# Optimization experiments

Measured on AMD Instinct MI355X. Metric: run time of the kernel, lower is better.

Reference implementation:

```python
import jax, jax.numpy as jnp
import numpy as np

N_NODES = 50000
N_EDGES = 800000
IN_DIM = 128
HID = 64
HEADS = 4
SLOPE = 0.01


def edge_softmax(e, dst, n):
    # e: [E, H] logits, softmax over edges sharing the same destination node
    m = jax.ops.segment_max(e, dst, num_segments=n)          # [N, H]
    ex = jnp.exp(e - m[dst])                                 # [E, H]
    s = jax.ops.segment_sum(ex, dst, num_segments=n)         # [N, H]
    return ex / s[dst]


def gat_conv(h, src, dst, W, attn_l, attn_r, bias, n, heads, out_dim):
    ft = (h @ W).reshape(n, heads, out_dim)                  # [N, H, D]
    el = jnp.sum(ft * attn_l, axis=-1)                       # [N, H]
    er = jnp.sum(ft * attn_r, axis=-1)                       # [N, H]
    e = jax.nn.leaky_relu(el[src] + er[dst], SLOPE)          # [E, H]
    a = edge_softmax(e, dst, n)                              # [E, H]
    msg = ft[src] * a[:, :, None]                            # [E, H, D]
    out = jax.ops.segment_sum(msg, dst, num_segments=n)      # [N, H, D]
    return out + bias.reshape(1, heads, out_dim)


def setup_inputs() -> dict:
    key = jax.random.key(0)
    ks = jax.random.split(key, 12)
    inputs = jax.random.normal(ks[0], (N_NODES, IN_DIM), dtype=jnp.float32)
    src = jax.random.randint(ks[1], (N_EDGES,), 0, N_NODES, dtype=jnp.int32)
    dst = jax.random.randint(ks[2], (N_EDGES,), 0, N_NODES, dtype=jnp.int32)
    s1 = 1.0 / np.sqrt(IN_DIM)
    W1 = jax.random.normal(ks[3], (IN_DIM, HEADS * HID), dtype=jnp.float32) * s1
    al1 = jax.random.normal(ks[4], (HEADS, HID), dtype=jnp.float32) * 0.1
    ar1 = jax.random.normal(ks[5], (HEADS, HID), dtype=jnp.float32) * 0.1
    b1 = jnp.zeros((HEADS * HID,), dtype=jnp.float32)
    s2 = 1.0 / np.sqrt(HEADS * HID)
    W2 = jax.random.normal(ks[6], (HEADS * HID, HID), dtype=jnp.float32) * s2
    al2 = jax.random.normal(ks[7], (1, HID), dtype=jnp.float32) * 0.1
    ar2 = jax.random.normal(ks[8], (1, HID), dtype=jnp.float32) * 0.1
    b2 = jnp.zeros((HID,), dtype=jnp.float32)
    return {"inputs": inputs, "src": src, "dst": dst,
            "W1": W1, "al1": al1, "ar1": ar1, "b1": b1,
            "W2": W2, "al2": al2, "ar2": ar2, "b2": b2}


def reference(inputs, src, dst, W1, al1, ar1, b1, W2, al2, ar2, b2):
    # layer 1: multi-head, activation elu, flatten heads
    h = gat_conv(inputs, src, dst, W1, al1, ar1, b1, N_NODES, HEADS, HID)
    h = jax.nn.elu(h).reshape(N_NODES, HEADS * HID)
    # layer 2 (last): single head
    h = gat_conv(h, src, dst, W2, al2, ar2, b2, N_NODES, 1, HID)
    h = jax.nn.elu(h).reshape(N_NODES, HID)
    return h
```

## Files before the change

### kernel.cpp

```cpp
#include <hip/hip_runtime.h>
#include <hip/hip_bf16.h>
#include <math.h>

#define N_NODES 50000
#define N_EDGES 800000
#define IN_DIM 128
#define HID 64
#define HEADS 4

typedef unsigned short ushort_t;
typedef __attribute__((ext_vector_type(8))) short bf16x8;
typedef __attribute__((ext_vector_type(4))) float f32x4;

static __device__ __forceinline__ ushort_t f2bf(float f) {
  __hip_bfloat16 b = __float2bfloat16(f);
  return *(ushort_t*)&b;
}
static __device__ __forceinline__ float bflo(unsigned d) {
  union { unsigned u; float f; } c; c.u = d << 16; return c.f;
}
static __device__ __forceinline__ float bfhi(unsigned d) {
  union { unsigned u; float f; } c; c.u = d & 0xffff0000u; return c.f;
}
static __device__ __forceinline__ unsigned packbf(float lo, float hi) {
  return (unsigned)f2bf(lo) | ((unsigned)f2bf(hi) << 16);
}
static __device__ __forceinline__ float lrelu(float x) {
  return (x > 0.f) ? x : 0.01f * x;
}

__global__ __launch_bounds__(256) void k_cvt_hist(const float* __restrict__ w1,
                                                  const float* __restrict__ w2,
                                                  ushort_t* __restrict__ bpk1,
                                                  ushort_t* __restrict__ bpk2,
                                                  const int* __restrict__ dst,
                                                  int* __restrict__ cnt) {
  constexpr int NP1 = 4096;
  constexpr int NP2 = 2048;
  constexpr int CVT_BLK = (NP1 + NP2) / 256;
  int bid = blockIdx.x;
  if (bid < CVT_BLK) {
    int t = bid * 256 + threadIdx.x;
    if (t < NP1) {
      int l = t & 63, rem = t >> 6;
      int kk = rem & 3, ct = (rem >> 2) & 3, hh = rem >> 4;
      int kb = kk * 32 + (l >> 4) * 8;
      int col = hh * 64 + ct * 16 + (l & 15);
      ushort_t v[8];
      #pragma unroll
      for (int j = 0; j < 8; ++j) v[j] = f2bf(w1[(kb + j) * 256 + col]);
      *(uint4*)&bpk1[t * 8] = *(uint4*)v;
    } else {
      int u = t - NP1;
      int l = u & 63, rem = u >> 6;
      int kk = rem & 7, ct = rem >> 3;
      int kb = kk * 32 + (l >> 4) * 8;
      int col = ct * 16 + (l & 15);
      ushort_t v[8];
      #pragma unroll
      for (int j = 0; j < 8; ++j) v[j] = f2bf(w2[(kb + j) * 64 + col]);
      *(uint4*)&bpk2[u * 8] = *(uint4*)v;
    }
  } else {
    int e = (bid - CVT_BLK) * 256 + threadIdx.x;
    if (e < N_EDGES) atomicAdd(&cnt[dst[e]], 1);
  }
}

__global__ __launch_bounds__(512) void k_scan_gemm1(const int* __restrict__ cnt,
                                                    int* __restrict__ offp,
                                                    int* __restrict__ bsum,
                                                    const float* __restrict__ A,
                                                    const ushort_t* __restrict__ Bpk,
                                                    ushort_t* __restrict__ C,
                                                    const float* __restrict__ al,
                                                    const float* __restrict__ ar,
                                                    float* __restrict__ el,
                                                    float* __restrict__ er, int M) {
  __shared__ char smraw[128 * 40 * 2];
  const int tid = threadIdx.x;
  if (blockIdx.x < 49) {
    int* lds = (int*)smraw;
    int i = blockIdx.x * 1024 + tid * 2;
    int v0 = (i < N_NODES) ? cnt[i] : 0;
    int v1 = (i + 1 < N_NODES) ? cnt[i + 1] : 0;
    int t = v0 + v1;
    lds[tid] = t;
    __syncthreads();
    for (int s = 1; s < 512; s <<= 1) {
      int u = (tid >= s) ? lds[tid - s] : 0;
      __syncthreads();
      lds[tid] += u;
      __syncthreads();
    }
    int excl = lds[tid] - t;
    if (i < N_NODES) offp[i] = excl;
    if (i + 1 < N_NODES) offp[i + 1] = excl + v0;
    if (tid == 511) bsum[blockIdx.x] = lds[511];
    return;
  }
  ushort_t (*As)[40] = (ushort_t(*)[40])smraw;
  const int m0 = (blockIdx.x - 49) * 128;
  const int w = tid >> 6, l = tid & 63;
  const int hh = w >> 1, rh = (w & 1) * 64;
  const int lr = l & 15, lk = l >> 4;
  f32x4 acc[4][4] = {};

  #pragma unroll
  for (int kk = 0; kk < 4; ++kk) {
    int k0 = kk * 32;
    {
      int r = tid >> 2, kc = (tid & 3) * 8;
      float4 va = make_float4(0.f, 0.f, 0.f, 0.f), vb = va;
      if (m0 + r < M) {
        va = *(const float4*)&A[(size_t)(m0 + r) * IN_DIM + k0 + kc];
        vb = *(const float4*)&A[(size_t)(m0 + r) * IN_DIM + k0 + kc + 4];
      }
      uint4 p;
      p.x = packbf(va.x, va.y); p.y = packbf(va.z, va.w);
      p.z = packbf(vb.x, vb.y); p.w = packbf(vb.z, vb.w);
      *(uint4*)&As[r][kc] = p;
    }
    __syncthreads();
    bf16x8 a[4];
    #pragma unroll
    for (int rt = 0; rt < 4; ++rt) a[rt] = *(const bf16x8*)&As[rh + rt * 16 + lr][lk * 8];
    #pragma unroll
    for (int ct = 0; ct < 4; ++ct) {
      bf16x8 b = ((const bf16x8*)Bpk)[((hh * 4 + ct) * 4 + kk) * 64 + l];
      #pragma unroll
      for (int rt = 0; rt < 4; ++rt)
        acc[rt][ct] = __builtin_amdgcn_mfma_f32_16x16x32_bf16(a[rt], b, acc[rt][ct], 0, 0, 0);
    }
    __syncthreads();
  }
  float ala[4], ara[4];
  #pragma unroll
  for (int ct = 0; ct < 4; ++ct) {
    ala[ct] = al[hh * 64 + ct * 16 + lr];
    ara[ct] = ar[hh * 64 + ct * 16 + lr];
  }
  #pragma unroll
  for (int rt = 0; rt < 4; ++rt)
    #pragma unroll
    for (int j = 0; j < 4; ++j) {
      float pel = 0.f, per = 0.f;
      #pragma unroll
      for (int ct = 0; ct < 4; ++ct) {
        float v = acc[rt][ct][j];
        pel = fmaf(v, ala[ct], pel);
        per = fmaf(v, ara[ct], per);
      }
      #pragma unroll
      for (int o = 1; o <= 8; o <<= 1) {
        pel += __shfl_xor(pel, o);
        per += __shfl_xor(per, o);
      }
      int row = m0 + rh + rt * 16 + lk * 4 + j;
      if (lr == 0 && row < M) { el[row * 4 + hh] = pel; er[row * 4 + hh] = per; }
    }
  #pragma unroll
  for (int rt = 0; rt < 4; ++rt)
    #pragma unroll
    for (int ct = 0; ct < 4; ++ct)
      #pragma unroll
      for (int j = 0; j < 4; ++j) {
        int row = m0 + rh + rt * 16 + lk * 4 + j;
        if (row < M) C[(size_t)row * 256 + hh * 64 + ct * 16 + lr] = f2bf(acc[rt][ct][j]);
      }
}

__global__ __launch_bounds__(256) void k_off_place(const int* __restrict__ offp,
                                                   const int* __restrict__ bsum,
                                                   int* __restrict__ off,
                                                   const int* __restrict__ src,
                                                   const int* __restrict__ dst,
                                                   int* __restrict__ cnt2,
                                                   int* __restrict__ ssrc) {
  __shared__ int pref[64];
  const int tid = threadIdx.x;
  const int bid = blockIdx.x;
  if (bid < 49) {
    if (tid < 64) {
      int v = (tid < bid) ? bsum[tid] : 0;
      #pragma unroll
      for (int o = 1; o < 64; o <<= 1) v += __shfl_xor(v, o);
      if (tid == 0) pref[0] = v;
    }
    __syncthreads();
    int e0 = pref[0];
    int i = bid * 1024 + tid * 4;
    if (i + 3 < N_NODES) {
      int4 q = *(const int4*)&offp[i];
      *(int4*)&off[i] = make_int4(q.x + e0, q.y + e0, q.z + e0, q.w + e0);
    } else {
      if (i < N_NODES) off[i] = offp[i] + e0;
      if (i + 1 < N_NODES) off[i + 1] = offp[i + 1] + e0;
      if (i + 2 < N_NODES) off[i + 2] = offp[i + 2] + e0;
      if (i + 3 < N_NODES) off[i + 3] = offp[i + 3] + e0;
    }
    if (bid == 0 && tid == 0) off[N_NODES] = N_EDGES;
    return;
  }
  if (tid < 64) {
    int v = (tid < 49) ? bsum[tid] : 0;
    int orig = v;
    #pragma unroll
    for (int o = 1; o < 64; o <<= 1) { int u = __shfl_up(v, o); if (tid >= o) v += u; }
    pref[tid] = v - orig;
  }
  __syncthreads();
  int e = (bid - 49) * 256 + tid;
  if (e < N_EDGES) {
    int d = dst[e];
    int p = atomicAdd(&cnt2[d], 1);
    ssrc[offp[d] + pref[d >> 10] + p] = src[e];
  }
}

__global__ __launch_bounds__(256) void agg4f_k(const ushort_t* __restrict__ ftb,
                                               const float* __restrict__ el,
                                               const float* __restrict__ er,
                                               const int* __restrict__ off,
                                               const int* __restrict__ ssrc,
                                               const float* __restrict__ bias,
                                               ushort_t* __restrict__ outb) {
  __shared__ float wl[4][64][4];
  __shared__ int srcl[4][64];
  int wv = threadIdx.x >> 6, lane = threadIdx.x & 63;
  int n = blockIdx.x * 4 + wv;
  if (n >= N_NODES) return;
  int s0 = off[n], s1 = off[n + 1];
  int half = lane >> 5, sl = lane & 31;
  int head = sl >> 3;
  const float4* el4 = (const float4*)el;
  float4 erv = ((const float4*)er)[n];
  float4 sum = make_float4(0.f, 0.f, 0.f, 0.f);
  float acc[8] = {};
  for (int c = s0; c < s1; c += 64) {
    int e = c + lane;
    float4 ex = make_float4(0.f, 0.f, 0.f, 0.f);
    int s = 0;
    if (e < s1) {
      s = ssrc[e];
      float4 q = el4[s];
      ex.x = __expf(lrelu(q.x + erv.x));
      ex.y = __expf(lrelu(q.y + erv.y));
      ex.z = __expf(lrelu(q.z + erv.z));
      ex.w = __expf(lrelu(q.w + erv.w));
      sum.x += ex.x; sum.y += ex.y; sum.z += ex.z; sum.w += ex.w;
    }
    srcl[wv][lane] = s;
    *(float4*)&wl[wv][lane][0] = ex;
    int cend = (c + 64 < s1) ? c + 64 : s1;
    #pragma unroll 4
    for (int i = c; i < cend; i += 2) {
      int e2 = i + half;
      if (e2 < cend) {
        int idx = e2 - c;
        int ss = srcl[wv][idx];
        float w = wl[wv][idx][head];
        uint4 u = *(const uint4*)&ftb[ss * 256 + sl * 8];
        acc[0] = fmaf(w, bflo(u.x), acc[0]);
        acc[1] = fmaf(w, bfhi(u.x), acc[1]);
        acc[2] = fmaf(w, bflo(u.y), acc[2]);
        acc[3] = fmaf(w, bfhi(u.y), acc[3]);
        acc[4] = fmaf(w, bflo(u.z), acc[4]);
        acc[5] = fmaf(w, bfhi(u.z), acc[5]);
        acc[6] = fmaf(w, bflo(u.w), acc[6]);
        acc[7] = fmaf(w, bfhi(u.w), acc[7]);
      }
    }
  }
  #pragma unroll
  for (int o = 1; o <= 32; o <<= 1) {
    sum.x += __shfl_xor(sum.x, o); sum.y += __shfl_xor(sum.y, o);
    sum.z += __shfl_xor(sum.z, o); sum.w += __shfl_xor(sum.w, o);
  }
  #pragma unroll
  for (int j = 0; j < 8; ++j) acc[j] += __shfl_xor(acc[j], 32);
  if (half == 0) {
    float sd = (head == 0) ? sum.x : (head == 1) ? sum.y : (head == 2) ? sum.z : sum.w;
    float rsv = (s1 > s0) ? 1.f / sd : 0.f;
    float4 b0 = ((const float4*)bias)[sl * 2];
    float4 b1 = ((const float4*)bias)[sl * 2 + 1];
    float o[8] = {fmaf(acc[0], rsv, b0.x), fmaf(acc[1], rsv, b0.y),
                  fmaf(acc[2], rsv, b0.z), fmaf(acc[3], rsv, b0.w),
                  fmaf(acc[4], rsv, b1.x), fmaf(acc[5], rsv, b1.y),
                  fmaf(acc[6], rsv, b1.z), fmaf(acc[7], rsv, b1.w)};
    #pragma unroll
    for (int j = 0; j < 8; ++j) o[j] = (o[j] > 0.f) ? o[j] : expm1f(o[j]);
    uint4 p;
    p.x = packbf(o[0], o[1]); p.y = packbf(o[2], o[3]);
    p.z = packbf(o[4], o[5]); p.w = packbf(o[6], o[7]);
    *(uint4*)&outb[n * 256 + sl * 8] = p;
  }
}

__global__ __launch_bounds__(512) void gemm2_mfma(const ushort_t* __restrict__ A,
                                                  const ushort_t* __restrict__ Bpk,
                                                  ushort_t* __restrict__ C,
                                                  const float* __restrict__ al,
                                                  const float* __restrict__ ar,
                                                  float* __restrict__ el,
                                                  float* __restrict__ er, int M) {
  __shared__ ushort_t As[128][40];
  const int tid = threadIdx.x;
  const int m0 = blockIdx.x * 128;
  const int w = tid >> 6, l = tid & 63;
  const int lr = l & 15, lk = l >> 4;
  f32x4 acc[4] = {};

  #pragma unroll
  for (int kk = 0; kk < 8; ++kk) {
    int k0 = kk * 32;
    {
      int r = tid >> 2, kc = (tid & 3) * 8;
      uint4 v = make_uint4(0, 0, 0, 0);
      if (m0 + r < M) v = *(const uint4*)&A[(size_t)(m0 + r) * 256 + k0 + kc];
      *(uint4*)&As[r][kc] = v;
    }
    __syncthreads();
    bf16x8 a = *(const bf16x8*)&As[w * 16 + lr][lk * 8];
    #pragma unroll
    for (int ct = 0; ct < 4; ++ct) {
      bf16x8 b = ((const bf16x8*)Bpk)[(ct * 8 + kk) * 64 + l];
      acc[ct] = __builtin_amdgcn_mfma_f32_16x16x32_bf16(a, b, acc[ct], 0, 0, 0);
    }
    __syncthreads();
  }
  float ala[4], ara[4];
  #pragma unroll
  for (int ct = 0; ct < 4; ++ct) {
    ala[ct] = al[ct * 16 + lr];
    ara[ct] = ar[ct * 16 + lr];
  }
  #pragma unroll
  for (int j = 0; j < 4; ++j) {
    float pel = 0.f, per = 0.f;
    #pragma unroll
    for (int ct = 0; ct < 4; ++ct) {
      float v = acc[ct][j];
      pel = fmaf(v, ala[ct], pel);
      per = fmaf(v, ara[ct], per);
    }
    #pragma unroll
    for (int o = 1; o <= 8; o <<= 1) {
      pel += __shfl_xor(pel, o);
      per += __shfl_xor(per, o);
    }
    int row = m0 + w * 16 + lk * 4 + j;
    if (lr == 0 && row < M) { el[row] = pel; er[row] = per; }
  }
  #pragma unroll
  for (int ct = 0; ct < 4; ++ct)
    #pragma unroll
    for (int j = 0; j < 4; ++j) {
      int row = m0 + w * 16 + lk * 4 + j;
      if (row < M) C[(size_t)row * 64 + ct * 16 + lr] = f2bf(acc[ct][j]);
    }
}

__global__ __launch_bounds__(256) void agg1f_k(const ushort_t* __restrict__ ftb,
                                               const float* __restrict__ el,
                                               const float* __restrict__ er,
                                               const int* __restrict__ off,
                                               const int* __restrict__ ssrc,
                                               const float* __restrict__ bias,
                                               float* __restrict__ out) {
  __shared__ float wl[4][64];
  __shared__ int srcl[4][64];
  int wv = threadIdx.x >> 6, lane = threadIdx.x & 63;
  int n = blockIdx.x * 4 + wv;
  if (n >= N_NODES) return;
  int s0 = off[n], s1 = off[n + 1];
  int g = lane >> 3, cg = lane & 7;
  float erv = er[n];
  float sum = 0.f;
  float acc[8] = {};
  for (int c = s0; c < s1; c += 64) {
    int e = c + lane;
    float ex = 0.f;
    int s = 0;
    if (e < s1) {
      s = ssrc[e];
      ex = __expf(lrelu(el[s] + erv));
      sum += ex;
    }
    srcl[wv][lane] = s;
    wl[wv][lane] = ex;
    int cend = (c + 64 < s1) ? c + 64 : s1;
    #pragma unroll 2
    for (int i = c; i < cend; i += 8) {
      int e2 = i + g;
      if (e2 < cend) {
        int idx = e2 - c;
        int ss = srcl[wv][idx];
        float w = wl[wv][idx];
        uint4 u = *(const uint4*)&ftb[ss * 64 + cg * 8];
        acc[0] = fmaf(w, bflo(u.x), acc[0]);
        acc[1] = fmaf(w, bfhi(u.x), acc[1]);
        acc[2] = fmaf(w, bflo(u.y), acc[2]);
        acc[3] = fmaf(w, bfhi(u.y), acc[3]);
        acc[4] = fmaf(w, bflo(u.z), acc[4]);
        acc[5] = fmaf(w, bfhi(u.z), acc[5]);
        acc[6] = fmaf(w, bflo(u.w), acc[6]);
        acc[7] = fmaf(w, bfhi(u.w), acc[7]);
      }
    }
  }
  #pragma unroll
  for (int o = 1; o <= 32; o <<= 1) sum += __shfl_xor(sum, o);
  #pragma unroll
  for (int o = 8; o <= 32; o <<= 1)
    #pragma unroll
    for (int j = 0; j < 8; ++j) acc[j] += __shfl_xor(acc[j], o);
  if (g == 0) {
    float rsv = (s1 > s0) ? 1.f / sum : 0.f;
    float4 b0 = ((const float4*)bias)[cg * 2];
    float4 b1 = ((const float4*)bias)[cg * 2 + 1];
    float o[8] = {fmaf(acc[0], rsv, b0.x), fmaf(acc[1], rsv, b0.y),
                  fmaf(acc[2], rsv, b0.z), fmaf(acc[3], rsv, b0.w),
                  fmaf(acc[4], rsv, b1.x), fmaf(acc[5], rsv, b1.y),
                  fmaf(acc[6], rsv, b1.z), fmaf(acc[7], rsv, b1.w)};
    #pragma unroll
    for (int j = 0; j < 8; ++j) o[j] = (o[j] > 0.f) ? o[j] : expm1f(o[j]);
    float4* out4 = (float4*)out;
    out4[(size_t)n * 16 + cg * 2]     = make_float4(o[0], o[1], o[2], o[3]);
    out4[(size_t)n * 16 + cg * 2 + 1] = make_float4(o[4], o[5], o[6], o[7]);
  }
}

extern "C" void kernel_launch(void* const* d_in, const int* in_sizes, int n_in,
                              void* d_out, int out_size, void* d_ws, size_t ws_size,
                              hipStream_t stream) {
  const float* x   = (const float*)d_in[0];
  const int*   src = (const int*)d_in[1];
  const int*   dst = (const int*)d_in[2];
  const float* W1  = (const float*)d_in[3];
  const float* al1 = (const float*)d_in[4];
  const float* ar1 = (const float*)d_in[5];
  const float* b1  = (const float*)d_in[6];
  const float* W2  = (const float*)d_in[7];
  const float* al2 = (const float*)d_in[8];
  const float* ar2 = (const float*)d_in[9];
  const float* b2  = (const float*)d_in[10];
  float* out = (float*)d_out;

  char* ws = (char*)d_ws;
  size_t wo = 0;
  auto alloc = [&](size_t b) { void* p = ws + wo; wo = (wo + b + 255) & ~(size_t)255; return p; };
  ushort_t* ft1b = (ushort_t*)alloc((size_t)N_NODES * 256 * 2);
  ushort_t* h1b  = (ushort_t*)alloc((size_t)N_NODES * 256 * 2);
  ushort_t* bpk1 = (ushort_t*)alloc((size_t)IN_DIM * 256 * 2);
  ushort_t* bpk2 = (ushort_t*)alloc((size_t)256 * 64 * 2);
  float* el1 = (float*)alloc((size_t)N_NODES * 4 * 4);
  float* er1 = (float*)alloc((size_t)N_NODES * 4 * 4);
  int*   off = (int*)alloc((size_t)(N_NODES + 1) * 4);
  int*   offp= (int*)alloc((size_t)N_NODES * 4);
  int*   cntp= (int*)alloc((size_t)2 * N_NODES * 4);
  int*   bsum= (int*)alloc(256);
  int*   ssrc= (int*)alloc((size_t)N_EDGES * 4);
  int* cnt  = cntp;
  int* cnt2 = cntp + N_NODES;
  ushort_t* ft2b = ft1b;
  float* el2 = el1, *er2 = er1;

  hipMemsetAsync(cntp, 0, (size_t)2 * N_NODES * 4, stream);
  k_cvt_hist<<<24 + 3125, 256, 0, stream>>>(W1, W2, bpk1, bpk2, dst, cnt);
  k_scan_gemm1<<<49 + 391, 512, 0, stream>>>(cnt, offp, bsum,
                                             x, bpk1, ft1b, al1, ar1, el1, er1, N_NODES);
  k_off_place<<<49 + 3125, 256, 0, stream>>>(offp, bsum, off, src, dst, cnt2, ssrc);
  agg4f_k<<<(N_NODES + 3) / 4, 256, 0, stream>>>(ft1b, el1, er1, off, ssrc, b1, h1b);
  gemm2_mfma<<<391, 512, 0, stream>>>(h1b, bpk2, ft2b, al2, ar2, el2, er2, N_NODES);
  agg1f_k<<<(N_NODES + 3) / 4, 256, 0, stream>>>(ft2b, el2, er2, off, ssrc, b2, out);
}
```

Measured before the change: 228.3 us.

## Fuse preprocessing and first GEMM into persistent kernel with grid barriers

Replaces three launches (weight conversion plus histogram, scan plus GEMM1, offset plus placement) with one persistent 512-block kernel that uses software grid barriers between phases. The GEMM1 tile shrinks to 32 rows with 256 threads, so it can interleave with edge placement. The scan is reworked to 4 elements per thread. The aim is to remove kernel launch gaps and tail effects. In exchange it adds spin-barrier overhead and relies on all 512 blocks being co-resident.

```diff
diff --git a/kernel.cpp b/kernel.cpp
--- a/kernel.cpp
+++ b/kernel.cpp
@@ -7,6 +7,7 @@
 #define IN_DIM 128
 #define HID 64
 #define HEADS 4
+#define MEGA_NB 512
 
 typedef unsigned short ushort_t;
 typedef __attribute__((ext_vector_type(8))) short bf16x8;
@@ -29,192 +30,188 @@
   return (x > 0.f) ? x : 0.01f * x;
 }
 
-__global__ __launch_bounds__(256) void k_cvt_hist(const float* __restrict__ w1,
-                                                  const float* __restrict__ w2,
-                                                  ushort_t* __restrict__ bpk1,
-                                                  ushort_t* __restrict__ bpk2,
-                                                  const int* __restrict__ dst,
-                                                  int* __restrict__ cnt) {
-  constexpr int NP1 = 4096;
-  constexpr int NP2 = 2048;
-  constexpr int CVT_BLK = (NP1 + NP2) / 256;
-  int bid = blockIdx.x;
-  if (bid < CVT_BLK) {
-    int t = bid * 256 + threadIdx.x;
-    if (t < NP1) {
-      int l = t & 63, rem = t >> 6;
-      int kk = rem & 3, ct = (rem >> 2) & 3, hh = rem >> 4;
-      int kb = kk * 32 + (l >> 4) * 8;
-      int col = hh * 64 + ct * 16 + (l & 15);
-      ushort_t v[8];
-      #pragma unroll
-      for (int j = 0; j < 8; ++j) v[j] = f2bf(w1[(kb + j) * 256 + col]);
-      *(uint4*)&bpk1[t * 8] = *(uint4*)v;
+static __device__ __forceinline__ void grid_barrier(unsigned* bar, unsigned nb) {
+  __syncthreads();
+  if (threadIdx.x == 0) {
+    __threadfence();
+    __hip_atomic_fetch_add(bar, 1u, __ATOMIC_ACQ_REL, __HIP_MEMORY_SCOPE_AGENT);
+    while (__hip_atomic_load(bar, __ATOMIC_ACQUIRE, __HIP_MEMORY_SCOPE_AGENT) < nb)
+      __builtin_amdgcn_s_sleep(8);
+    __threadfence();
+  }
+  __syncthreads();
+}
+
+__global__ __launch_bounds__(256, 2) void k_mega(
+    const float* __restrict__ w1, const float* __restrict__ w2,
+    ushort_t* __restrict__ bpk1, ushort_t* __restrict__ bpk2,
+    const int* __restrict__ dst, const int* __restrict__ src,
+    int* __restrict__ cnt, int* __restrict__ cnt2, unsigned* __restrict__ bar,
+    int* __restrict__ offp, int* __restrict__ bsum, int* __restrict__ off,
+    int* __restrict__ ssrc,
+    const float* __restrict__ A, ushort_t* __restrict__ C,
+    const float* __restrict__ al, const float* __restrict__ ar,
+    float* __restrict__ el, float* __restrict__ er) {
+  __shared__ char smraw[2816];
+  const int tid = threadIdx.x;
+  const unsigned nb = gridDim.x;
+
+  for (int u = blockIdx.x; u < 24 + 3125; u += MEGA_NB) {
+    if (u < 24) {
+      int t = u * 256 + tid;
+      if (t < 4096) {
+        int l = t & 63, rem = t >> 6;
+        int kk = rem & 3, ct = (rem >> 2) & 3, hh = rem >> 4;
+        int kb = kk * 32 + (l >> 4) * 8;
+        int col = hh * 64 + ct * 16 + (l & 15);
+        ushort_t v[8];
+        #pragma unroll
+        for (int j = 0; j < 8; ++j) v[j] = f2bf(w1[(kb + j) * 256 + col]);
+        *(uint4*)&bpk1[t * 8] = *(uint4*)v;
+      } else {
+        int q = t - 4096;
+        int l = q & 63, rem = q >> 6;
+        int kk = rem & 7, ct = rem >> 3;
+        int kb = kk * 32 + (l >> 4) * 8;
+        int col = ct * 16 + (l & 15);
+        ushort_t v[8];
+        #pragma unroll
+        for (int j = 0; j < 8; ++j) v[j] = f2bf(w2[(kb + j) * 64 + col]);
+        *(uint4*)&bpk2[q * 8] = *(uint4*)v;
+      }
     } else {
-      int u = t - NP1;
-      int l = u & 63, rem = u >> 6;
-      int kk = rem & 7, ct = rem >> 3;
-      int kb = kk * 32 + (l >> 4) * 8;
-      int col = ct * 16 + (l & 15);
-      ushort_t v[8];
-      #pragma unroll
-      for (int j = 0; j < 8; ++j) v[j] = f2bf(w2[(kb + j) * 64 + col]);
-      *(uint4*)&bpk2[u * 8] = *(uint4*)v;
-    }
-  } else {
-    int e = (bid - CVT_BLK) * 256 + threadIdx.x;
-    if (e < N_EDGES) atomicAdd(&cnt[dst[e]], 1);
-  }
-}
-
-__global__ __launch_bounds__(512) void k_scan_gemm1(const int* __restrict__ cnt,
-                                                    int* __restrict__ offp,
-                                                    int* __restrict__ bsum,
-                                                    const float* __restrict__ A,
-                                                    const ushort_t* __restrict__ Bpk,
-                                                    ushort_t* __restrict__ C,
-                                                    const float* __restrict__ al,
-                                                    const float* __restrict__ ar,
-                                                    float* __restrict__ el,
-                                                    float* __restrict__ er, int M) {
-  __shared__ char smraw[128 * 40 * 2];
-  const int tid = threadIdx.x;
-  if (blockIdx.x < 49) {
+      int e = (u - 24) * 256 + tid;
+      if (e < N_EDGES) atomicAdd(&cnt[dst[e]], 1);
+    }
+  }
+  grid_barrier(&bar[0], nb);
+
+  for (int u = blockIdx.x; u < 49; u += MEGA_NB) {
     int* lds = (int*)smraw;
-    int i = blockIdx.x * 1024 + tid * 2;
-    int v0 = (i < N_NODES) ? cnt[i] : 0;
-    int v1 = (i + 1 < N_NODES) ? cnt[i + 1] : 0;
-    int t = v0 + v1;
+    int i = u * 1024 + tid * 4;
+    int v0 = 0, v1 = 0, v2 = 0, v3 = 0;
+    if (i + 3 < N_NODES) {
+      int4 q = *(const int4*)&cnt[i];
+      v0 = q.x; v1 = q.y; v2 = q.z; v3 = q.w;
+    } else {
+      if (i < N_NODES) v0 = cnt[i];
+      if (i + 1 < N_NODES) v1 = cnt[i + 1];
+      if (i + 2 < N_NODES) v2 = cnt[i + 2];
+      if (i + 3 < N_NODES) v3 = cnt[i + 3];
+    }
+    int t = v0 + v1 + v2 + v3;
     lds[tid] = t;
     __syncthreads();
-    for (int s = 1; s < 512; s <<= 1) {
-      int u = (tid >= s) ? lds[tid - s] : 0;
+    for (int s = 1; s < 256; s <<= 1) {
+      int u2 = (tid >= s) ? lds[tid - s] : 0;
       __syncthreads();
-      lds[tid] += u;
+      lds[tid] += u2;
       __syncthreads();
     }
     int excl = lds[tid] - t;
     if (i < N_NODES) offp[i] = excl;
     if (i + 1 < N_NODES) offp[i + 1] = excl + v0;
-    if (tid == 511) bsum[blockIdx.x] = lds[511];
-    return;
-  }
-  ushort_t (*As)[40] = (ushort_t(*)[40])smraw;
-  const int m0 = (blockIdx.x - 49) * 128;
-  const int w = tid >> 6, l = tid & 63;
-  const int hh = w >> 1, rh = (w & 1) * 64;
-  const int lr = l & 15, lk = l >> 4;
-  f32x4 acc[4][4] = {};
-
-  #pragma unroll
-  for (int kk = 0; kk < 4; ++kk) {
-    int k0 = kk * 32;
-    {
-      int r = tid >> 2, kc = (tid & 3) * 8;
-      float4 va = make_float4(0.f, 0.f, 0.f, 0.f), vb = va;
-      if (m0 + r < M) {
-        va = *(const float4*)&A[(size_t)(m0 + r) * IN_DIM + k0 + kc];
-        vb = *(const float4*)&A[(size_t)(m0 + r) * IN_DIM + k0 + kc + 4];
-      }
-      uint4 p;
-      p.x = packbf(va.x, va.y); p.y = packbf(va.z, va.w);
-      p.z = packbf(vb.x, vb.y); p.w = packbf(vb.z, vb.w);
-      *(uint4*)&As[r][kc] = p;
-    }
+    if (i + 2 < N_NODES) offp[i + 2] = excl + v0 + v1;
+    if (i + 3 < N_NODES) offp[i + 3] = excl + v0 + v1 + v2;
+    if (tid == 255) bsum[u] = lds[255];
     __syncthreads();
-    bf16x8 a[4];
-    #pragma unroll
-    for (int rt = 0; rt < 4; ++rt) a[rt] = *(const bf16x8*)&As[rh + rt * 16 + lr][lk * 8];
-    #pragma unroll
-    for (int ct = 0; ct < 4; ++ct) {
-      bf16x8 b = ((const bf16x8*)Bpk)[((hh * 4 + ct) * 4 + kk) * 64 + l];
-      #pragma unroll
-      for (int rt = 0; rt < 4; ++rt)
-        acc[rt][ct] = __builtin_amdgcn_mfma_f32_16x16x32_bf16(a[rt], b, acc[rt][ct], 0, 0, 0);
-    }
-    __syncthreads();
-  }
-  float ala[4], ara[4];
-  #pragma unroll
-  for (int ct = 0; ct < 4; ++ct) {
-    ala[ct] = al[hh * 64 + ct * 16 + lr];
-    ara[ct] = ar[hh * 64 + ct * 16 + lr];
-  }
-  #pragma unroll
-  for (int rt = 0; rt < 4; ++rt)
-    #pragma unroll
-    for (int j = 0; j < 4; ++j) {
-      float pel = 0.f, per = 0.f;
-      #pragma unroll
-      for (int ct = 0; ct < 4; ++ct) {
-        float v = acc[rt][ct][j];
-        pel = fmaf(v, ala[ct], pel);
-        per = fmaf(v, ara[ct], per);
-      }
-      #pragma unroll
-      for (int o = 1; o <= 8; o <<= 1) {
-        pel += __shfl_xor(pel, o);
-        per += __shfl_xor(per, o);
-      }
-      int row = m0 + rh + rt * 16 + lk * 4 + j;
-      if (lr == 0 && row < M) { el[row * 4 + hh] = pel; er[row * 4 + hh] = per; }
-    }
-  #pragma unroll
-  for (int rt = 0; rt < 4; ++rt)
-    #pragma unroll
-    for (int ct = 0; ct < 4; ++ct)
-      #pragma unroll
-      for (int j = 0; j < 4; ++j) {
-        int row = m0 + rh + rt * 16 + lk * 4 + j;
-        if (row < M) C[(size_t)row * 256 + hh * 64 + ct * 16 + lr] = f2bf(acc[rt][ct][j]);
-      }
-}
-
-__global__ __launch_bounds__(256) void k_off_place(const int* __restrict__ offp,
-                                                   const int* __restrict__ bsum,
-                                                   int* __restrict__ off,
-                                                   const int* __restrict__ src,
-                                                   const int* __restrict__ dst,
-                                                   int* __restrict__ cnt2,
-                                                   int* __restrict__ ssrc) {
-  __shared__ int pref[64];
-  const int tid = threadIdx.x;
-  const int bid = blockIdx.x;
-  if (bid < 49) {
-    if (tid < 64) {
-      int v = (tid < bid) ? bsum[tid] : 0;
-      #pragma unroll
-      for (int o = 1; o < 64; o <<= 1) v += __shfl_xor(v, o);
-      if (tid == 0) pref[0] = v;
-    }
-    __syncthreads();
-    int e0 = pref[0];
-    int i = bid * 1024 + tid * 4;
-    if (i + 3 < N_NODES) {
-      int4 q = *(const int4*)&offp[i];
-      *(int4*)&off[i] = make_int4(q.x + e0, q.y + e0, q.z + e0, q.w + e0);
-    } else {
-      if (i < N_NODES) off[i] = offp[i] + e0;
-      if (i + 1 < N_NODES) off[i + 1] = offp[i + 1] + e0;
-      if (i + 2 < N_NODES) off[i + 2] = offp[i + 2] + e0;
-      if (i + 3 < N_NODES) off[i + 3] = offp[i + 3] + e0;
-    }
-    if (bid == 0 && tid == 0) off[N_NODES] = N_EDGES;
-    return;
-  }
+  }
+  grid_barrier(&bar[1], nb);
+
+  int* pref = (int*)(smraw + 2560);
   if (tid < 64) {
     int v = (tid < 49) ? bsum[tid] : 0;
     int orig = v;
     #pragma unroll
-    for (int o = 1; o < 64; o <<= 1) { int u = __shfl_up(v, o); if (tid >= o) v += u; }
+    for (int o = 1; o < 64; o <<= 1) { int t2 = __shfl_up(v, o); if (tid >= o) v += t2; }
     pref[tid] = v - orig;
   }
   __syncthreads();
-  int e = (bid - 49) * 256 + tid;
-  if (e < N_EDGES) {
-    int d = dst[e];
-    int p = atomicAdd(&cnt2[d], 1);
-    ssrc[offp[d] + pref[d >> 10] + p] = src[e];
+
+  ushort_t (*As)[40] = (ushort_t(*)[40])smraw;
+  for (int u = blockIdx.x; u < 3125 + 1563 + 49; u += MEGA_NB) {
+    if (u < 3125) {
+      int e = u * 256 + tid;
+      if (e < N_EDGES) {
+        int d = dst[e];
+        int p = atomicAdd(&cnt2[d], 1);
+        ssrc[offp[d] + pref[d >> 10] + p] = src[e];
+      }
+    } else if (u < 3125 + 1563) {
+      int m0 = (u - 3125) * 32;
+      const int w = tid >> 6, l = tid & 63;
+      const int lr = l & 15, lk = l >> 4;
+      f32x4 acc[2][4] = {};
+      #pragma unroll
+      for (int kk = 0; kk < 4; ++kk) {
+        {
+          int r = tid >> 3, kc = (tid & 7) * 4;
+          float4 v = make_float4(0.f, 0.f, 0.f, 0.f);
+          if (m0 + r < N_NODES) v = *(const float4*)&A[(size_t)(m0 + r) * IN_DIM + kk * 32 + kc];
+          *(uint2*)&As[r][kc] = make_uint2(packbf(v.x, v.y), packbf(v.z, v.w));
+        }
+        __syncthreads();
+        bf16x8 a0 = *(const bf16x8*)&As[lr][lk * 8];
+        bf16x8 a1 = *(const bf16x8*)&As[16 + lr][lk * 8];
+        #pragma unroll
+        for (int ct = 0; ct < 4; ++ct) {
+          bf16x8 b = ((const bf16x8*)bpk1)[((w * 4 + ct) * 4 + kk) * 64 + l];
+          acc[0][ct] = __builtin_amdgcn_mfma_f32_16x16x32_bf16(a0, b, acc[0][ct], 0, 0, 0);
+          acc[1][ct] = __builtin_amdgcn_mfma_f32_16x16x32_bf16(a1, b, acc[1][ct], 0, 0, 0);
+        }
+        __syncthreads();
+      }
+      float ala[4], ara[4];
+      #pragma unroll
+      for (int ct = 0; ct < 4; ++ct) {
+        ala[ct] = al[w * 64 + ct * 16 + lr];
+        ara[ct] = ar[w * 64 + ct * 16 + lr];
+      }
+      #pragma unroll
+      for (int rt = 0; rt < 2; ++rt)
+        #pragma unroll
+        for (int j = 0; j < 4; ++j) {
+          float pel = 0.f, per = 0.f;
+          #pragma unroll
+          for (int ct = 0; ct < 4; ++ct) {
+            float v = acc[rt][ct][j];
+            pel = fmaf(v, ala[ct], pel);
+            per = fmaf(v, ara[ct], per);
+          }
+          #pragma unroll
+          for (int o = 1; o <= 8; o <<= 1) {
+            pel += __shfl_xor(pel, o);
+            per += __shfl_xor(per, o);
+          }
+          int row = m0 + rt * 16 + lk * 4 + j;
+          if (lr == 0 && row < N_NODES) { el[row * 4 + w] = pel; er[row * 4 + w] = per; }
+        }
+      #pragma unroll
+      for (int rt = 0; rt < 2; ++rt)
+        #pragma unroll
+        for (int ct = 0; ct < 4; ++ct)
+          #pragma unroll
+          for (int j = 0; j < 4; ++j) {
+            int row = m0 + rt * 16 + lk * 4 + j;
+            if (row < N_NODES)
+              C[(size_t)row * 256 + w * 64 + ct * 16 + lr] = f2bf(acc[rt][ct][j]);
+          }
+    } else {
+      int b2 = u - (3125 + 1563);
+      int e0 = pref[b2];
+      int i = b2 * 1024 + tid * 4;
+      if (i + 3 < N_NODES) {
+        int4 q = *(const int4*)&offp[i];
+        *(int4*)&off[i] = make_int4(q.x + e0, q.y + e0, q.z + e0, q.w + e0);
+      } else {
+        if (i < N_NODES) off[i] = offp[i] + e0;
+        if (i + 1 < N_NODES) off[i + 1] = offp[i + 1] + e0;
+        if (i + 2 < N_NODES) off[i + 2] = offp[i + 2] + e0;
+        if (i + 3 < N_NODES) off[i + 3] = offp[i + 3] + e0;
+      }
+      if (b2 == 0 && tid == 0) off[N_NODES] = N_EDGES;
+    }
+    __syncthreads();
   }
 }
 
@@ -458,19 +455,20 @@
   float* er1 = (float*)alloc((size_t)N_NODES * 4 * 4);
   int*   off = (int*)alloc((size_t)(N_NODES + 1) * 4);
   int*   offp= (int*)alloc((size_t)N_NODES * 4);
-  int*   cntp= (int*)alloc((size_t)2 * N_NODES * 4);
+  size_t zbytes = (size_t)2 * N_NODES * 4 + 256;
+  int*   zz  = (int*)alloc(zbytes);
   int*   bsum= (int*)alloc(256);
   int*   ssrc= (int*)alloc((size_t)N_EDGES * 4);
-  int* cnt  = cntp;
-  int* cnt2 = cntp + N_NODES;
+  int* cnt  = zz;
+  int* cnt2 = zz + N_NODES;
+  unsigned* bar = (unsigned*)(zz + 2 * N_NODES);
   ushort_t* ft2b = ft1b;
   float* el2 = el1, *er2 = er1;
 
-  hipMemsetAsync(cntp, 0, (size_t)2 * N_NODES * 4, stream);
-  k_cvt_hist<<<24 + 3125, 256, 0, stream>>>(W1, W2, bpk1, bpk2, dst, cnt);
-  k_scan_gemm1<<<49 + 391, 512, 0, stream>>>(cnt, offp, bsum,
-                                             x, bpk1, ft1b, al1, ar1, el1, er1, N_NODES);
-  k_off_place<<<49 + 3125, 256, 0, stream>>>(offp, bsum, off, src, dst, cnt2, ssrc);
+  hipMemsetAsync(zz, 0, zbytes, stream);
+  k_mega<<<MEGA_NB, 256, 0, stream>>>(W1, W2, bpk1, bpk2, dst, src,
+                                      cnt, cnt2, bar, offp, bsum, off, ssrc,
+                                      x, ft1b, al1, ar1, el1, er1);
   agg4f_k<<<(N_NODES + 3) / 4, 256, 0, stream>>>(ft1b, el1, er1, off, ssrc, b1, h1b);
   gemm2_mfma<<<391, 512, 0, stream>>>(h1b, bpk2, ft2b, al2, ar2, el2, er2, N_NODES);
   agg1f_k<<<(N_NODES + 3) / 4, 256, 0, stream>>>(ft2b, el2, er2, off, ssrc, b2, out);
```

Result: slower. 332.1 us (+45.5%).
